# Optimization experiments

Hardware: AMD Instinct MI355X
Metric: run time of the kernel (lower is better)

## Reference

```python
import jax, jax.numpy as jnp
import numpy as np

B = 32
NEG_INF = -1e30


def _conv2d(x, w, b):
    # x: (B,C,H,W), w: (O,I,kh,kw), VALID, stride 1
    y = jax.lax.conv_general_dilated(x, w, (1, 1), 'VALID',
                                     dimension_numbers=('NCHW', 'OIHW', 'NCHW'))
    return y + b[None, :, None, None]


def _maxpool_3_2_1(x):
    return jax.lax.reduce_window(x, NEG_INF, jax.lax.max,
                                 (1, 1, 3, 3), (1, 1, 2, 2),
                                 ((0, 0), (0, 0), (1, 1), (1, 1)))


def _extract_patches(x, kh, kw, stride):
    # x: (B,C,H,W) -> (B,C,oh,kh,ow,kw)
    H, W = x.shape[2], x.shape[3]
    oh = (H - kh) // stride + 1
    ow = (W - kw) // stride + 1
    rows = jnp.arange(oh)[:, None] * stride + jnp.arange(kh)[None, :]  # (oh,kh)
    cols = jnp.arange(ow)[:, None] * stride + jnp.arange(kw)[None, :]  # (ow,kw)
    return x[:, :, rows][:, :, :, :, cols]  # (B,C,oh,kh,ow,kw)


def _local_conv(x, w, b, stride):
    # unshared-weight conv. w: (oh,ow,oc,ic,kh,kw), b: (oc,oh,ow)
    kh, kw = w.shape[4], w.shape[5]
    p = _extract_patches(x, kh, kw, stride)              # (B,ic,oh,kh,ow,kw)
    y = jnp.einsum('bcpkql,pqockl->bopq', p, w)          # (B,oc,oh,ow)
    return y + b[None]


def setup_inputs() -> dict:
    key = jax.random.key(0)
    ks = jax.random.split(key, 14)
    s = 0.05
    f32 = jnp.float32
    inp = {
        'x': jax.random.normal(ks[0], (B, 3, 152, 152), dtype=f32),
        'conv1_w': jax.random.normal(ks[1], (32, 3, 11, 11), dtype=f32) * s,
        'conv1_b': jax.random.normal(ks[2], (32,), dtype=f32) * s,
        'conv2_w': jax.random.normal(ks[3], (16, 32, 9, 9), dtype=f32) * s,
        'conv2_b': jax.random.normal(ks[4], (16,), dtype=f32) * s,
        'lc1_w': jax.random.normal(ks[5], (55, 55, 16, 16, 9, 9), dtype=f32) * s,
        'lc1_b': jax.random.normal(ks[6], (16, 55, 55), dtype=f32) * s,
        'lc2_w': jax.random.normal(ks[7], (25, 25, 16, 16, 7, 7), dtype=f32) * s,
        'lc2_b': jax.random.normal(ks[8], (16, 25, 25), dtype=f32) * s,
        'lc3_w': jax.random.normal(ks[9], (21, 21, 16, 16, 5, 5), dtype=f32) * s,
        'lc3_b': jax.random.normal(ks[10], (16, 21, 21), dtype=f32) * s,
        'fc1_w': jax.random.normal(ks[11], (4096, 16 * 21 * 21), dtype=f32) * s,
        'fc1_b': jax.random.normal(ks[12], (4096,), dtype=f32) * s,
    }
    return inp


def reference(x, conv1_w, conv1_b, conv2_w, conv2_b,
              lc1_w, lc1_b, lc2_w, lc2_b, lc3_w, lc3_b,
              fc1_w, fc1_b):
    h = jax.nn.relu(_conv2d(x, conv1_w, conv1_b))        # (B,32,142,142)
    h = _maxpool_3_2_1(h)                                # (B,32,71,71)
    h = jax.nn.relu(_conv2d(h, conv2_w, conv2_b))        # (B,16,63,63)
    h = jax.nn.relu(_local_conv(h, lc1_w, lc1_b, 1))     # (B,16,55,55)
    h = jax.nn.relu(_local_conv(h, lc2_w, lc2_b, 2))     # (B,16,25,25)
    h = jax.nn.relu(_local_conv(h, lc3_w, lc3_b, 1))     # (B,16,21,21)
    h = h.reshape(h.shape[0], 16 * 21 * 21)
    return h @ fc1_w.T + fc1_b                           # (B,4096)
```

## Files before the change

kernel.cpp:

```cpp
#include <hip/hip_runtime.h>
#include <cstddef>

typedef __attribute__((ext_vector_type(8))) short bf16x8;
typedef __attribute__((ext_vector_type(8), aligned(8))) short bf16x8a;
typedef __attribute__((ext_vector_type(4))) float f32x4;
typedef __attribute__((ext_vector_type(4))) unsigned short u16x4;
typedef __attribute__((ext_vector_type(8))) unsigned short u16x8;

__device__ inline unsigned short f2bf(float f) {
  unsigned int u = __float_as_uint(f);
  unsigned int r = (u + 0x7FFFu + ((u >> 16) & 1u)) >> 16;
  return (unsigned short)r;
}
__device__ inline float bf2f(unsigned short u) {
  return __uint_as_float((unsigned int)u << 16);
}

__device__ inline int xcd_swz(int bid, int nwg) {
  const int xcd = bid & 7;
  const int idx = bid >> 3;
  const int q = nwg >> 3, r = nwg & 7;
  return (xcd < r) ? xcd * (q + 1) + idx : r * (q + 1) + (xcd - r) * q + idx;
}

__global__ __launch_bounds__(256) void prep_x1w1(const float* __restrict__ x,
                                                 const float* __restrict__ w,
                                                 unsigned short* __restrict__ xb,
                                                 unsigned short* __restrict__ wb) {
  if (blockIdx.x < 3040) {
    const int j = blockIdx.x * 256 + threadIdx.x;
    const int iw = j % 160;
    const int ih = (j / 160) % 152;
    const int b = j / (160 * 152);
    unsigned short v[4] = {0, 0, 0, 0};
    if (iw < 152) {
      #pragma unroll
      for (int ic = 0; ic < 3; ++ic)
        v[ic] = f2bf(x[(size_t)(b * 3 + ic) * 23104 + ih * 152 + iw]);
    }
    *(unsigned long long*)(xb + ((((size_t)ih * 160 + iw) * 32) + b) * 4) =
        *(unsigned long long*)v;
  } else {
    const int j = (blockIdx.x - 3040) * 256 + threadIdx.x;
    const int e = j & 7;
    const int s = (j >> 3) & 31;
    const int kcj = j >> 8;
    const int kc = kcj & 3, step = kcj >> 2;
    const int t = step * 8 + kc * 2 + (e >> 2);
    const int ics = e & 3;
    const int kh = t / 12, kwp = t - kh * 12;
    float val = 0.f;
    if (t < 132 && kwp < 11 && ics < 3)
      val = w[((s * 3 + ics) * 11 + kh) * 11 + kwp];
    wb[j] = f2bf(val);
  }
}

__global__ __launch_bounds__(256) void conv1_mfma(const unsigned short* __restrict__ xb,
                                                  const unsigned short* __restrict__ wb,
                                                  const float* __restrict__ bias,
                                                  unsigned short* __restrict__ outB) {
  __shared__ unsigned short xs[11 * 19 * 128];
  const int tile = blockIdx.x;
  const int oh = blockIdx.y;
  const int ow0 = min(tile * 8, 134);
  const int tid = threadIdx.x;

  for (int ch = tid; ch < 3344; ch += 256) {
    const int e = ch & 15;
    const int pix = ch >> 4;
    const int c = pix % 19, r = pix / 19;
    *(u16x8*)(xs + (size_t)pix * 128 + e * 8) =
        *(const u16x8*)(xb + (((size_t)(oh + r) * 160) + (ow0 + c)) * 128 + e * 8);
  }
  __syncthreads();

  const int lane = tid & 63, wvi = tid >> 6;
  const int row = lane & 15;
  const int kc = lane >> 4;
  f32x4 acc[2][4];
  #pragma unroll
  for (int p = 0; p < 2; ++p)
    #pragma unroll
    for (int q = 0; q < 4; ++q) acc[p][q] = (f32x4){0.f, 0.f, 0.f, 0.f};

  #pragma unroll 2
  for (int j = 0; j < 17; ++j) {
    const int t0 = j * 8 + 2 * kc;
    int kh = t0 / 12;
    int kwp = t0 - kh * 12;
    if (t0 >= 132) { kh = 0; kwp = 0; }
    const bf16x8 wa0 = *(const bf16x8*)(wb + (((j * 4 + kc) * 32) + row) * 8);
    const bf16x8 wa1 = *(const bf16x8*)(wb + (((j * 4 + kc) * 32) + 16 + row) * 8);
    #pragma unroll
    for (int p = 0; p < 2; ++p) {
      const int cl = wvi + p * 4 + kwp;
      const unsigned short* xp = xs + (kh * 19 + cl) * 128 + row * 4;
      bf16x8 xv0, xv1;
      ((unsigned long long*)&xv0)[0] = *(const unsigned long long*)(xp);
      ((unsigned long long*)&xv0)[1] = *(const unsigned long long*)(xp + 128);
      ((unsigned long long*)&xv1)[0] = *(const unsigned long long*)(xp + 64);
      ((unsigned long long*)&xv1)[1] = *(const unsigned long long*)(xp + 192);
      acc[p][0] = __builtin_amdgcn_mfma_f32_16x16x32_bf16(wa0, xv0, acc[p][0], 0, 0, 0);
      acc[p][1] = __builtin_amdgcn_mfma_f32_16x16x32_bf16(wa0, xv1, acc[p][1], 0, 0, 0);
      acc[p][2] = __builtin_amdgcn_mfma_f32_16x16x32_bf16(wa1, xv0, acc[p][2], 0, 0, 0);
      acc[p][3] = __builtin_amdgcn_mfma_f32_16x16x32_bf16(wa1, xv1, acc[p][3], 0, 0, 0);
    }
  }

  #pragma unroll
  for (int p = 0; p < 2; ++p) {
    const int pos = oh * 142 + ow0 + wvi + p * 4;
    unsigned short* ob = outB + (size_t)pos * 1024;
    u16x4 p00, p01, p10, p11;
    #pragma unroll
    for (int r = 0; r < 4; ++r) {
      const float bv0 = bias[kc * 4 + r];
      const float bv1 = bias[16 + kc * 4 + r];
      p00[r] = f2bf(fmaxf(acc[p][0][r] + bv0, 0.f));
      p01[r] = f2bf(fmaxf(acc[p][1][r] + bv0, 0.f));
      p10[r] = f2bf(fmaxf(acc[p][2][r] + bv1, 0.f));
      p11[r] = f2bf(fmaxf(acc[p][3][r] + bv1, 0.f));
    }
    *(u16x4*)(ob + row * 32 + kc * 4) = p00;
    *(u16x4*)(ob + (row + 16) * 32 + kc * 4) = p01;
    *(u16x4*)(ob + row * 32 + 16 + kc * 4) = p10;
    *(u16x4*)(ob + (row + 16) * 32 + 16 + kc * 4) = p11;
  }
}

__global__ __launch_bounds__(256) void poolt2_wb2(const unsigned short* __restrict__ in,
                                                  unsigned short* __restrict__ xb,
                                                  const float* __restrict__ w2,
                                                  unsigned short* __restrict__ wb2) {
  if (blockIdx.x < 631) {
    const int tid = threadIdx.x;
    const int b = tid & 31, pg = tid >> 5;
    const int posp = blockIdx.x * 8 + pg;
    if (posp >= 5041) return;
    const int ohp = posp / 71, owp = posp % 71;
    u16x8 m[4];
    #pragma unroll
    for (int q = 0; q < 4; ++q)
      #pragma unroll
      for (int e = 0; e < 8; ++e) m[q][e] = 0;

    #pragma unroll
    for (int kh = 0; kh < 3; ++kh) {
      const int ih = ohp * 2 - 1 + kh;
      if (ih < 0 || ih >= 142) continue;
      #pragma unroll
      for (int kw = 0; kw < 3; ++kw) {
        const int iw = owp * 2 - 1 + kw;
        if (iw < 0 || iw >= 142) continue;
        const u16x8* p =
            (const u16x8*)(in + (((size_t)(ih * 142 + iw)) * 32 + b) * 32);
        #pragma unroll
        for (int q = 0; q < 4; ++q) {
          const u16x8 v = p[q];
          #pragma unroll
          for (int e = 0; e < 8; ++e) m[q][e] = (v[e] > m[q][e]) ? v[e] : m[q][e];
        }
      }
    }
    u16x8* o = (u16x8*)(xb + ((size_t)posp * 32 + b) * 32);
    #pragma unroll
    for (int q = 0; q < 4; ++q) o[q] = m[q];
  } else {
    const int j = (blockIdx.x - 631) * 256 + threadIdx.x;
    const int ic = j & 31, oc = (j >> 5) & 15, sp = j >> 9;
    wb2[j] = f2bf(w2[(size_t)oc * 2592 + ic * 81 + sp]);
  }
}

__global__ __launch_bounds__(256) void conv2_mfma(const unsigned short* __restrict__ xb,
                                                  const unsigned short* __restrict__ wb,
                                                  const float* __restrict__ bias,
                                                  unsigned short* __restrict__ outB) {
  const int lane = threadIdx.x & 63;
  const int wvi = threadIdx.x >> 6;
  const int bid = xcd_swz(blockIdx.x, 993);
  int pos = bid * 4 + wvi;
  if (pos > 3968) pos = 3968;
  const int oh = pos / 63, ow = pos % 63;
  const int row = lane & 15;
  const int kc = lane >> 4;
  f32x4 acc0 = {0.f, 0.f, 0.f, 0.f}, acc1 = {0.f, 0.f, 0.f, 0.f};
  const unsigned short* xbase = xb + (size_t)(oh * 71 + ow) * 1024;
  const int aoff = row * 32 + kc * 8;
  const int boff0 = aoff;
  const int boff1 = (row + 16) * 32 + kc * 8;

  #pragma unroll
  for (int g = 0; g < 20; ++g) {
    bf16x8 A[4], Ba[4], Bb[4];
    #pragma unroll
    for (int i = 0; i < 4; ++i) {
      const int sp = g * 4 + i;
      const int kh = sp / 9, kw = sp - kh * 9;
      A[i] = *(const bf16x8*)(wb + sp * 512 + aoff);
      const unsigned short* xp = xbase + (kh * 71 + kw) * 1024;
      Ba[i] = *(const bf16x8*)(xp + boff0);
      Bb[i] = *(const bf16x8*)(xp + boff1);
    }
    #pragma unroll
    for (int i = 0; i < 4; ++i) {
      acc0 = __builtin_amdgcn_mfma_f32_16x16x32_bf16(A[i], Ba[i], acc0, 0, 0, 0);
      acc1 = __builtin_amdgcn_mfma_f32_16x16x32_bf16(A[i], Bb[i], acc1, 0, 0, 0);
    }
  }
  {
    const bf16x8 a = *(const bf16x8*)(wb + 80 * 512 + aoff);
    const unsigned short* xp = xbase + (8 * 71 + 8) * 1024;
    const bf16x8 b0 = *(const bf16x8*)(xp + boff0);
    const bf16x8 b1 = *(const bf16x8*)(xp + boff1);
    acc0 = __builtin_amdgcn_mfma_f32_16x16x32_bf16(a, b0, acc0, 0, 0, 0);
    acc1 = __builtin_amdgcn_mfma_f32_16x16x32_bf16(a, b1, acc1, 0, 0, 0);
  }

  u16x4 pk0, pk1;
  #pragma unroll
  for (int r = 0; r < 4; ++r) {
    const float bv = bias[kc * 4 + r];
    pk0[r] = f2bf(fmaxf(acc0[r] + bv, 0.f));
    pk1[r] = f2bf(fmaxf(acc1[r] + bv, 0.f));
  }
  *(u16x4*)(outB + (size_t)pos * 512 + row * 16 + kc * 4) = pk0;
  *(u16x4*)(outB + (size_t)pos * 512 + (row + 16) * 16 + kc * 4) = pk1;
}

__global__ __launch_bounds__(256) void prep_lcw_all(const float* __restrict__ w1,
                                                    unsigned short* __restrict__ o1,
                                                    const float* __restrict__ w2,
                                                    unsigned short* __restrict__ o2,
                                                    const float* __restrict__ w3,
                                                    unsigned short* __restrict__ o3) {
  __shared__ float ls[8 * 16 * 81];
  int blk = blockIdx.x;
  const float* wp;
  unsigned short* ob;
  int KHW;
  if (blk < 3025) {
    KHW = 81; wp = w1 + (size_t)blk * 256 * 81; ob = o1 + (size_t)blk * 41 * 512;
  } else if (blk < 3650) {
    blk -= 3025;
    KHW = 49; wp = w2 + (size_t)blk * 256 * 49; ob = o2 + (size_t)blk * 25 * 512;
  } else {
    blk -= 3650;
    KHW = 25; wp = w3 + (size_t)blk * 256 * 25; ob = o3 + (size_t)blk * 13 * 512;
  }
  const int P = (KHW + 1) / 2;
  const int tid = threadIdx.x;

  for (int half = 0; half < 2; ++half) {
    __syncthreads();
    for (int j = tid; j < 8 * 16 * KHW; j += 256)
      ls[j] = wp[half * (8 * 16 * KHW) + j];
    __syncthreads();
    for (int j = tid; j < P * 256; j += 256) {
      const int ic = j & 15, tl = (j >> 4) & 1, oc8 = (j >> 5) & 7, pair = j >> 8;
      const int tap = pair * 2 + tl;
      const float v = (tap < KHW) ? ls[(oc8 * 16 + ic) * KHW + tap] : 0.f;
      ob[(size_t)pair * 512 + (half * 8 + oc8) * 32 + tl * 16 + ic] = f2bf(v);
    }
  }
}

template <int KH, int S, int IH, int OH>
__global__ __launch_bounds__(256) void lc_mfma(const unsigned short* __restrict__ xb,
                                               const unsigned short* __restrict__ wbT,
                                               const float* __restrict__ bias,
                                               unsigned short* __restrict__ out,
                                               int pos_count) {
  constexpr int KHW = KH * KH;
  constexpr int P = (KHW + 1) / 2;
  constexpr int NPOS = OH * OH;
  const int lane = threadIdx.x & 63;
  const int wvi = threadIdx.x >> 6;
  const int bid = xcd_swz(blockIdx.x, gridDim.x);
  int lpos = bid * 4 + wvi;
  if (lpos >= pos_count) lpos = pos_count - 1;
  const int pos = lpos;
  const int oh = pos / OH, ow = pos % OH;
  const int bcol = lane & 15;
  const int kc = lane >> 4;
  const int tsel = kc >> 1;
  const int icoff = (kc & 1) * 8;
  f32x4 acc0 = {0.f, 0.f, 0.f, 0.f}, acc1 = {0.f, 0.f, 0.f, 0.f};
  const unsigned short* wp = wbT + (size_t)lpos * (P * 512) + bcol * 32 + kc * 8;
  const int xorg = (oh * S) * IH + ow * S;

  #pragma unroll
  for (int g = 0; g < P / 4; ++g) {
    bf16x8 A[4], Ba[4], Bb[4];
    #pragma unroll
    for (int i = 0; i < 4; ++i) {
      const int p = g * 4 + i;
      const int t0 = 2 * p, t1 = 2 * p + 1;
      const int o0 = (t0 / KH) * IH + (t0 % KH);
      const int o1 = (t1 / KH) * IH + (t1 % KH);
      const int osel = tsel ? o1 : o0;
      A[i] = *(const bf16x8*)(wp + p * 512);
      const unsigned short* xp = xb + (size_t)(xorg + osel) * 512 + icoff;
      Ba[i] = *(const bf16x8*)(xp + bcol * 16);
      Bb[i] = *(const bf16x8*)(xp + (bcol + 16) * 16);
    }
    #pragma unroll
    for (int i = 0; i < 4; ++i) {
      acc0 = __builtin_amdgcn_mfma_f32_16x16x32_bf16(A[i], Ba[i], acc0, 0, 0, 0);
      acc1 = __builtin_amdgcn_mfma_f32_16x16x32_bf16(A[i], Bb[i], acc1, 0, 0, 0);
    }
  }
  {
    constexpr int p = P - 1;
    const int t0 = 2 * p;
    const int o0 = (t0 / KH) * IH + (t0 % KH);
    const bf16x8 a = *(const bf16x8*)(wp + p * 512);
    const unsigned short* xp = xb + (size_t)(xorg + o0) * 512 + icoff;
    const bf16x8 b0 = *(const bf16x8*)(xp + bcol * 16);
    const bf16x8 b1 = *(const bf16x8*)(xp + (bcol + 16) * 16);
    acc0 = __builtin_amdgcn_mfma_f32_16x16x32_bf16(a, b0, acc0, 0, 0, 0);
    acc1 = __builtin_amdgcn_mfma_f32_16x16x32_bf16(a, b1, acc1, 0, 0, 0);
  }

  u16x4 pk0, pk1;
  #pragma unroll
  for (int r = 0; r < 4; ++r) {
    const float bv = bias[(kc * 4 + r) * NPOS + pos];
    pk0[r] = f2bf(fmaxf(acc0[r] + bv, 0.f));
    pk1[r] = f2bf(fmaxf(acc1[r] + bv, 0.f));
  }
  *(u16x4*)(out + (size_t)pos * 512 + bcol * 16 + kc * 4) = pk0;
  *(u16x4*)(out + (size_t)pos * 512 + (bcol + 16) * 16 + kc * 4) = pk1;
}

__global__ __launch_bounds__(256) void fc_reformat2(const unsigned short* __restrict__ xb5,
                                                    float* __restrict__ xB) {
  const int j = blockIdx.x * 256 + threadIdx.x;
  const int k = j % 7056;
  const int b = j / 7056;
  const int oc = k / 441, pos = k % 441;
  xB[j] = bf2f(xb5[((size_t)pos * 32 + b) * 16 + oc]);
}

__global__ __launch_bounds__(256) void fc1_v5(const float* __restrict__ xB,
                                              const float* __restrict__ w,
                                              float* __restrict__ part) {
  const int lane = threadIdx.x & 63;
  const int b0 = (threadIdx.x >> 6) * 8;
  const int n0 = blockIdx.x * 8;
  const int kch = blockIdx.y;
  const int kbase = kch * 1764;
  float acc[8][8] = {};
  for (int it = 0; it < 7; ++it) {
    const int ko = it * 256 + lane * 4;
    const int kb = kbase + ko;
    float4 wf[8], xr[8];
    if (ko < 1764) {
      #pragma unroll
      for (int n = 0; n < 8; ++n)
        wf[n] = *(const float4*)&w[(size_t)(n0 + n) * 7056 + kb];
      #pragma unroll
      for (int bb = 0; bb < 8; ++bb)
        xr[bb] = *(const float4*)&xB[(size_t)(b0 + bb) * 7056 + kb];
    } else {
      #pragma unroll
      for (int n = 0; n < 8; ++n) wf[n] = make_float4(0.f, 0.f, 0.f, 0.f);
      #pragma unroll
      for (int bb = 0; bb < 8; ++bb) xr[bb] = make_float4(0.f, 0.f, 0.f, 0.f);
    }
    #pragma unroll
    for (int n = 0; n < 8; ++n)
      #pragma unroll
      for (int bb = 0; bb < 8; ++bb) {
        acc[n][bb] += wf[n].x * xr[bb].x + wf[n].y * xr[bb].y +
                      wf[n].z * xr[bb].z + wf[n].w * xr[bb].w;
      }
  }
  #pragma unroll
  for (int n = 0; n < 8; ++n)
    #pragma unroll
    for (int c = 0; c < 8; ++c)
      #pragma unroll
      for (int m = 1; m < 64; m <<= 1)
        acc[n][c] += __shfl_xor(acc[n][c], m, 64);
  float val = 0.f;
  #pragma unroll
  for (int n = 0; n < 8; ++n)
    #pragma unroll
    for (int c = 0; c < 8; ++c)
      if (lane == n * 8 + c) val = acc[n][c];
  const int n_l = lane >> 3, b_l = lane & 7;
  part[(((size_t)kch * 4096 + n0 + n_l) * 32) + b0 + b_l] = val;
}

__global__ __launch_bounds__(256) void fc_combine(const float* __restrict__ part,
                                                  const float* __restrict__ bias,
                                                  float* __restrict__ out) {
  const int j = blockIdx.x * 256 + threadIdx.x;
  const int n = j & 4095, b = j >> 12;
  float v = bias[n];
  #pragma unroll
  for (int k = 0; k < 4; ++k) v += part[(((size_t)k * 4096 + n) * 32) + b];
  out[(size_t)b * 4096 + n] = v;
}

extern "C" void kernel_launch(void* const* d_in, const int* in_sizes, int n_in,
                              void* d_out, int out_size, void* d_ws, size_t ws_size,
                              hipStream_t stream) {
  const float* x       = (const float*)d_in[0];
  const float* conv1_w = (const float*)d_in[1];
  const float* conv1_b = (const float*)d_in[2];
  const float* conv2_w = (const float*)d_in[3];
  const float* conv2_b = (const float*)d_in[4];
  const float* lc1_w   = (const float*)d_in[5];
  const float* lc1_b   = (const float*)d_in[6];
  const float* lc2_w   = (const float*)d_in[7];
  const float* lc2_b   = (const float*)d_in[8];
  const float* lc3_w   = (const float*)d_in[9];
  const float* lc3_b   = (const float*)d_in[10];
  const float* fc1_w   = (const float*)d_in[11];
  const float* fc1_b   = (const float*)d_in[12];
  float* out = (float*)d_out;
  char* ws = (char*)d_ws;

  unsigned short* xb1  = (unsigned short*)(ws + 0);
  unsigned short* wb1  = (unsigned short*)(ws + 8388608);
  unsigned short* c1B  = (unsigned short*)(ws + 16777216);
  unsigned short* xb2  = (unsigned short*)(ws + 67108864);
  unsigned short* wb2  = (unsigned short*)(ws + 83886080);
  unsigned short* h2b  = (unsigned short*)(ws + 92274688);
  unsigned short* xb3  = (unsigned short*)(ws + 100663296);
  unsigned short* xb4  = (unsigned short*)(ws + 109051904);
  unsigned short* xb5  = (unsigned short*)(ws + 117440512);
  float* xB            = (float*)(ws + 125829120);
  float* fcp           = (float*)(ws + 134217728);
  unsigned short* wbT1 = (unsigned short*)(ws + 167772160);
  unsigned short* wbT2 = (unsigned short*)(ws + 301989888);
  unsigned short* wbT3 = (unsigned short*)(ws + 318767104);

  prep_x1w1<<<3108, 256, 0, stream>>>(x, conv1_w, xb1, wb1);
  conv1_mfma<<<dim3(18, 142), 256, 0, stream>>>(xb1, wb1, conv1_b, c1B);
  poolt2_wb2<<<793, 256, 0, stream>>>(c1B, xb2, conv2_w, wb2);
  conv2_mfma<<<993, 256, 0, stream>>>(xb2, wb2, conv2_b, h2b);

  prep_lcw_all<<<4091, 256, 0, stream>>>(lc1_w, wbT1, lc2_w, wbT2, lc3_w, wbT3);
  lc_mfma<9, 1, 63, 55><<<757, 256, 0, stream>>>(h2b, wbT1, lc1_b, xb3, 3025);
  lc_mfma<7, 2, 55, 25><<<157, 256, 0, stream>>>(xb3, wbT2, lc2_b, xb4, 625);
  lc_mfma<5, 1, 25, 21><<<111, 256, 0, stream>>>(xb4, wbT3, lc3_b, xb5, 441);

  fc_reformat2<<<882, 256, 0, stream>>>(xb5, xB);
  fc1_v5<<<dim3(512, 4), 256, 0, stream>>>(xB, fc1_w, fcp);
  fc_combine<<<512, 256, 0, stream>>>(fcp, fc1_b, out);
}
```

Before: 350.2 us.

## Fuse LC weight prep into input prep kernel and split into quarter blocks

Merges the separate local-conv weight reformat kernel into the first input/conv1-weight prep kernel, so the whole preprocessing runs as one launch at the start of the stream. Each weight block is split into four quarter-blocks of four output channels each. This replaces the two-pass loop with its double barrier and cuts shared memory per block, which should allow more resident blocks on the bandwidth-bound fp32-to-bf16 conversion of roughly 250 MB of weights. The lc2 launch grid is also doubled, which with the existing position clamping may only add redundant blocks that rewrite the same output.

```diff
diff --git a/kernel.cpp b/kernel.cpp
--- a/kernel.cpp
+++ b/kernel.cpp
@@ -23,12 +23,47 @@
   return (xcd < r) ? xcd * (q + 1) + idx : r * (q + 1) + (xcd - r) * q + idx;
 }
 
-__global__ __launch_bounds__(256) void prep_x1w1(const float* __restrict__ x,
-                                                 const float* __restrict__ w,
-                                                 unsigned short* __restrict__ xb,
-                                                 unsigned short* __restrict__ wb) {
-  if (blockIdx.x < 3040) {
-    const int j = blockIdx.x * 256 + threadIdx.x;
+__global__ __launch_bounds__(256) void lcw_prep(
+    const float* __restrict__ w1, unsigned short* __restrict__ o1,
+    const float* __restrict__ w2, unsigned short* __restrict__ o2,
+    const float* __restrict__ w3, unsigned short* __restrict__ o3,
+    const float* __restrict__ x, const float* __restrict__ w,
+    unsigned short* __restrict__ xb, unsigned short* __restrict__ wb) {
+  __shared__ float ls[4 * 16 * 81];
+  const int tid = threadIdx.x;
+
+  if (blockIdx.x < 16364) {
+    const int q = blockIdx.x & 3;
+    int blk = blockIdx.x >> 2;
+    const float* wp;
+    unsigned short* ob;
+    int KHW;
+    if (blk < 3025) {
+      KHW = 81; wp = w1 + (size_t)blk * 256 * 81; ob = o1 + (size_t)blk * 41 * 512;
+    } else if (blk < 3650) {
+      blk -= 3025;
+      KHW = 49; wp = w2 + (size_t)blk * 256 * 49; ob = o2 + (size_t)blk * 25 * 512;
+    } else {
+      blk -= 3650;
+      KHW = 25; wp = w3 + (size_t)blk * 256 * 25; ob = o3 + (size_t)blk * 13 * 512;
+    }
+    const int P = (KHW + 1) / 2;
+    wp += (size_t)q * 64 * KHW;
+    ob += q * 128;
+    for (int j = tid; j < 64 * KHW; j += 256) ls[j] = wp[j];
+    __syncthreads();
+    for (int j = tid; j < P * 128; j += 256) {
+      const int ic = j & 15, tl = (j >> 4) & 1, ocl = (j >> 5) & 3, pair = j >> 7;
+      const int tap = pair * 2 + tl;
+      const float v = (tap < KHW) ? ls[(ocl * 16 + ic) * KHW + tap] : 0.f;
+      ob[(size_t)pair * 512 + ocl * 32 + tl * 16 + ic] = f2bf(v);
+    }
+    return;
+  }
+
+  const int pblk = blockIdx.x - 16364;
+  if (pblk < 3040) {
+    const int j = pblk * 256 + tid;
     const int iw = j % 160;
     const int ih = (j / 160) % 152;
     const int b = j / (160 * 152);
@@ -41,7 +76,7 @@
     *(unsigned long long*)(xb + ((((size_t)ih * 160 + iw) * 32) + b) * 4) =
         *(unsigned long long*)v;
   } else {
-    const int j = (blockIdx.x - 3040) * 256 + threadIdx.x;
+    const int j = (pblk - 3040) * 256 + tid;
     const int e = j & 7;
     const int s = (j >> 3) & 31;
     const int kcj = j >> 8;
@@ -227,43 +262,6 @@
   }
   *(u16x4*)(outB + (size_t)pos * 512 + row * 16 + kc * 4) = pk0;
   *(u16x4*)(outB + (size_t)pos * 512 + (row + 16) * 16 + kc * 4) = pk1;
-}
-
-__global__ __launch_bounds__(256) void prep_lcw_all(const float* __restrict__ w1,
-                                                    unsigned short* __restrict__ o1,
-                                                    const float* __restrict__ w2,
-                                                    unsigned short* __restrict__ o2,
-                                                    const float* __restrict__ w3,
-                                                    unsigned short* __restrict__ o3) {
-  __shared__ float ls[8 * 16 * 81];
-  int blk = blockIdx.x;
-  const float* wp;
-  unsigned short* ob;
-  int KHW;
-  if (blk < 3025) {
-    KHW = 81; wp = w1 + (size_t)blk * 256 * 81; ob = o1 + (size_t)blk * 41 * 512;
-  } else if (blk < 3650) {
-    blk -= 3025;
-    KHW = 49; wp = w2 + (size_t)blk * 256 * 49; ob = o2 + (size_t)blk * 25 * 512;
-  } else {
-    blk -= 3650;
-    KHW = 25; wp = w3 + (size_t)blk * 256 * 25; ob = o3 + (size_t)blk * 13 * 512;
-  }
-  const int P = (KHW + 1) / 2;
-  const int tid = threadIdx.x;
-
-  for (int half = 0; half < 2; ++half) {
-    __syncthreads();
-    for (int j = tid; j < 8 * 16 * KHW; j += 256)
-      ls[j] = wp[half * (8 * 16 * KHW) + j];
-    __syncthreads();
-    for (int j = tid; j < P * 256; j += 256) {
-      const int ic = j & 15, tl = (j >> 4) & 1, oc8 = (j >> 5) & 7, pair = j >> 8;
-      const int tap = pair * 2 + tl;
-      const float v = (tap < KHW) ? ls[(oc8 * 16 + ic) * KHW + tap] : 0.f;
-      ob[(size_t)pair * 512 + (half * 8 + oc8) * 32 + tl * 16 + ic] = f2bf(v);
-    }
-  }
 }
 
 template <int KH, int S, int IH, int OH>
@@ -439,14 +437,14 @@
   unsigned short* wbT2 = (unsigned short*)(ws + 301989888);
   unsigned short* wbT3 = (unsigned short*)(ws + 318767104);
 
-  prep_x1w1<<<3108, 256, 0, stream>>>(x, conv1_w, xb1, wb1);
+  lcw_prep<<<19472, 256, 0, stream>>>(lc1_w, wbT1, lc2_w, wbT2, lc3_w, wbT3,
+                                      x, conv1_w, xb1, wb1);
   conv1_mfma<<<dim3(18, 142), 256, 0, stream>>>(xb1, wb1, conv1_b, c1B);
   poolt2_wb2<<<793, 256, 0, stream>>>(c1B, xb2, conv2_w, wb2);
   conv2_mfma<<<993, 256, 0, stream>>>(xb2, wb2, conv2_b, h2b);
 
-  prep_lcw_all<<<4091, 256, 0, stream>>>(lc1_w, wbT1, lc2_w, wbT2, lc3_w, wbT3);
   lc_mfma<9, 1, 63, 55><<<757, 256, 0, stream>>>(h2b, wbT1, lc1_b, xb3, 3025);
-  lc_mfma<7, 2, 55, 25><<<157, 256, 0, stream>>>(xb3, wbT2, lc2_b, xb4, 625);
+  lc_mfma<7, 2, 55, 25><<<313, 256, 0, stream>>>(xb3, wbT2, lc2_b, xb4, 625);
   lc_mfma<5, 1, 25, 21><<<111, 256, 0, stream>>>(xb4, wbT3, lc3_b, xb5, 441);
 
   fc_reformat2<<<882, 256, 0, stream>>>(xb5, xB);
```

Result: faster. 326.9 us (-6.7%).
